# Kernel tuning notes

Measured on AMD Instinct MI355X. Metric: run time of the kernel, lower is better.

The kernel has to match this reference:

```python
import jax, jax.numpy as jnp
import numpy as np

B, D, CIN, H, W = 2, 6, 3, 96, 96
DIM, NUM_HEADS, DEPTH = 144, 6, 2
WS = (2, 8, 8)   # window size (d, h, w)
SS = (1, 4, 4)   # shift size for odd blocks
HID = int(DIM * 2.0)
TBL = (2 * WS[0] - 1) * (2 * WS[1] - 1) * (2 * WS[2] - 1)  # 675
EPS = 1e-5


def _rpi(ws):
    # pairwise relative position index, same math as WindowAttention.get_position_index
    coords = np.stack(np.meshgrid(np.arange(ws[0]), np.arange(ws[1]), np.arange(ws[2]), indexing='ij'))
    cf = coords.reshape(3, -1).astype(np.int64)
    rc = (cf[:, :, None] - cf[:, None, :]).transpose(1, 2, 0)
    rc[..., 0] += ws[0] - 1
    rc[..., 1] += ws[1] - 1
    rc[..., 2] += ws[2] - 1
    rc[..., 0] *= (2 * ws[1] - 1) * (2 * ws[2] - 1)
    rc[..., 1] *= 2 * ws[2] - 1
    return rc.sum(-1)  # (N, N)


def _win_part_np(x, ws):
    b, d, h, w, c = x.shape
    x = x.reshape(b, d // ws[0], ws[0], h // ws[1], ws[1], w // ws[2], ws[2], c)
    return x.transpose(0, 1, 3, 5, 2, 4, 6, 7).reshape(-1, ws[0] * ws[1] * ws[2], c)


def _attn_mask(Dp, Hp, Wp, ws, ss):
    # static shift-window attention mask, same as compute_mask
    img = np.zeros((1, Dp, Hp, Wp, 1), np.float32)
    cnt = 0
    for d in (slice(-ws[0]), slice(-ws[0], -ss[0]), slice(-ss[0], None)):
        for h in (slice(-ws[1]), slice(-ws[1], -ss[1]), slice(-ss[1], None)):
            for w in (slice(-ws[2]), slice(-ws[2], -ss[2]), slice(-ss[2], None)):
                img[:, d, h, w, :] = cnt
                cnt += 1
    mw = _win_part_np(img, ws)[..., 0]  # (nW, N)
    am = mw[:, None, :] - mw[:, :, None]
    return np.where(am != 0, np.float32(-100.0), np.float32(0.0))


RPI = jnp.asarray(_rpi(WS))            # (N, N) int
MASK = jnp.asarray(_attn_mask(D, H, W, WS, SS))  # (nW, N, N)


def _ln(x, g, b):
    mu = jnp.mean(x, -1, keepdims=True)
    var = jnp.mean(jnp.square(x - mu), -1, keepdims=True)
    return (x - mu) * jax.lax.rsqrt(var + EPS) * g + b


def _win_part(x, ws):
    b, d, h, w, c = x.shape
    x = x.reshape(b, d // ws[0], ws[0], h // ws[1], ws[1], w // ws[2], ws[2], c)
    return x.transpose(0, 1, 3, 5, 2, 4, 6, 7).reshape(-1, ws[0] * ws[1] * ws[2], c)


def _win_rev(xw, ws, b, d, h, w):
    x = xw.reshape(b, d // ws[0], h // ws[1], w // ws[2], ws[0], ws[1], ws[2], -1)
    return x.transpose(0, 1, 4, 2, 5, 3, 6, 7).reshape(b, d, h, w, -1)


def _stl(x, i, shifted, params):
    # one Swin Transformer Layer; x: (B, D, H, W, C)
    n1g, n1b, qkvw, qkvb, rpb, projw, projb, n2g, n2b, fc1w, fc1b, fc2w, fc2b = params
    b, d, h, w, c = x.shape
    hd = c // NUM_HEADS
    scale = hd ** -0.5
    y = _ln(x, n1g[i], n1b[i])
    if shifted:
        y = jnp.roll(y, (-SS[0], -SS[1], -SS[2]), axis=(1, 2, 3))
    xw = _win_part(y, WS)  # (B_, N, C)
    B_, N, _ = xw.shape
    qkv = jnp.einsum('bnc,oc->bno', xw, qkvw[i]) + qkvb[i]
    qkv = qkv.reshape(B_, N, 3, NUM_HEADS, hd).transpose(2, 0, 3, 1, 4)
    q, k, v = qkv[0], qkv[1], qkv[2]
    attn = jnp.einsum('bhnd,bhmd->bhnm', q * scale, k)
    bias = rpb[i][RPI].transpose(2, 0, 1)  # (heads, N, N)
    attn = attn + bias[None]
    if shifted:
        nW = MASK.shape[0]
        attn = attn.reshape(B_ // nW, nW, NUM_HEADS, N, N) + MASK[None, :, None]
        attn = attn.reshape(B_, NUM_HEADS, N, N)
    attn = jax.nn.softmax(attn, axis=-1)
    out = jnp.einsum('bhnm,bhmd->bhnd', attn, v).transpose(0, 2, 1, 3).reshape(B_, N, c)
    out = jnp.einsum('bnc,oc->bno', out, projw[i]) + projb[i]
    y = _win_rev(out, WS, b, d, h, w)
    if shifted:
        y = jnp.roll(y, (SS[0], SS[1], SS[2]), axis=(1, 2, 3))
    x = x + y
    z = _ln(x, n2g[i], n2b[i])
    z = jnp.einsum('bdhwc,oc->bdhwo', z, fc1w[i]) + fc1b[i]
    z = jax.nn.gelu(z, approximate=False)
    z = jnp.einsum('bdhwo,co->bdhwc', z, fc2w[i]) + fc2b[i]
    return x + z


def setup_inputs() -> dict:
    key = jax.random.key(0)
    ks = jax.random.split(key, 8)
    s = 0.02
    return {
        'x': jax.random.normal(ks[0], (B, D, CIN, H, W), jnp.float32),
        'conv_w': jax.random.normal(ks[1], (DIM, CIN, 1, 3, 3), jnp.float32) * s,
        'conv_b': jnp.zeros((DIM,), jnp.float32),
        'ln0_g': jnp.ones((DIM,), jnp.float32),
        'ln0_b': jnp.zeros((DIM,), jnp.float32),
        'n1g': jnp.ones((DEPTH, DIM), jnp.float32),
        'n1b': jnp.zeros((DEPTH, DIM), jnp.float32),
        'qkvw': jax.random.normal(ks[2], (DEPTH, 3 * DIM, DIM), jnp.float32) * s,
        'qkvb': jnp.zeros((DEPTH, 3 * DIM), jnp.float32),
        'rpb': jax.random.normal(ks[3], (DEPTH, TBL, NUM_HEADS), jnp.float32) * s,
        'projw': jax.random.normal(ks[4], (DEPTH, DIM, DIM), jnp.float32) * s,
        'projb': jnp.zeros((DEPTH, DIM), jnp.float32),
        'n2g': jnp.ones((DEPTH, DIM), jnp.float32),
        'n2b': jnp.zeros((DEPTH, DIM), jnp.float32),
        'fc1w': jax.random.normal(ks[5], (DEPTH, HID, DIM), jnp.float32) * s,
        'fc1b': jnp.zeros((DEPTH, HID), jnp.float32),
        'fc2w': jax.random.normal(ks[6], (DEPTH, DIM, HID), jnp.float32) * s,
        'fc2b': jnp.zeros((DEPTH, DIM), jnp.float32),
        'lin_w': jax.random.normal(ks[7], (DIM, DIM), jnp.float32) * s,
        'lin_b': jnp.zeros((DIM,), jnp.float32),
        'ln1_g': jnp.ones((DIM,), jnp.float32),
        'ln1_b': jnp.zeros((DIM,), jnp.float32),
    }


def reference(x, conv_w, conv_b, ln0_g, ln0_b, n1g, n1b, qkvw, qkvb, rpb, projw, projb,
              n2g, n2b, fc1w, fc1b, fc2w, fc2b, lin_w, lin_b, ln1_g, ln1_b):
    # x: (n, d, c, h, w)
    y = x.transpose(0, 2, 1, 3, 4)  # n c d h w
    y = jax.lax.conv_general_dilated(
        y, conv_w, (1, 1, 1), [(0, 0), (1, 1), (1, 1)],
        dimension_numbers=('NCDHW', 'OIDHW', 'NCDHW')) + conv_b[None, :, None, None, None]
    y = y.transpose(0, 2, 3, 4, 1)  # n d h w c
    y = _ln(y, ln0_g, ln0_b)
    y = y.transpose(0, 4, 1, 2, 3)  # n c d h w
    params = (n1g, n1b, qkvw, qkvb, rpb, projw, projb, n2g, n2b, fc1w, fc1b, fc2w, fc2b)
    # RSTB (num_blocks = 1): residual group (STG of DEPTH STLs) + linear + skip
    f = y.transpose(0, 2, 3, 4, 1)  # b d h w c
    for i in range(DEPTH):
        f = _stl(f, i, i % 2 == 1, params)
    f = jnp.einsum('bdhwc,oc->bdhwo', f, lin_w) + lin_b
    y = y + f.transpose(0, 4, 1, 2, 3)
    # trailing LayerNorm and rearrange back to (n, d, c, h, w)
    out = _ln(y.transpose(0, 2, 3, 4, 1), ln1_g, ln1_b)
    return out.transpose(0, 1, 4, 2, 3)
```

## Files before the change

### kernel.cpp

```cpp
#include <hip/hip_runtime.h>
#include <math.h>

#define NTOK 110592
#define NWIN 864
#define TS   15925248

typedef unsigned short u16;
typedef unsigned int   u32;
typedef __attribute__((ext_vector_type(8))) short short8;
typedef __attribute__((ext_vector_type(4))) float float4v;

__device__ __forceinline__ float bf2f(u16 v) { return __uint_as_float(((u32)v) << 16); }
__device__ __forceinline__ u16 f2bf(float f) {
    u32 u = __float_as_uint(f);
    u32 r = u + 0x7fffu + ((u >> 16) & 1u);
    return (u16)(r >> 16);
}
__device__ __forceinline__ void unpack2(u32 u, float& lo, float& hi) {
    lo = __uint_as_float(u << 16);
    hi = __uint_as_float(u & 0xffff0000u);
}
__device__ __forceinline__ u32 pack2(float lo, float hi) {
    return (u32)f2bf(lo) | ((u32)f2bf(hi) << 16);
}
__device__ __forceinline__ float wave_sum(float v) {
    #pragma unroll
    for (int o = 32; o > 0; o >>= 1) v += __shfl_xor(v, o, 64);
    return v;
}

__device__ __forceinline__ void win_to_src(int tw, int shifted, int& sb, int& sd, int& sh, int& sw) {
    int n = tw & 127;
    int win = tw >> 7;
    int ww = win % 12;
    int wh = (win / 12) % 12;
    int rest = win / 144;
    int wd = rest % 3;
    sb = rest / 3;
    int ld = n >> 6, lh = (n >> 3) & 7, lw = n & 7;
    int dr = wd * 2 + ld, hr = wh * 8 + lh, wr = ww * 8 + lw;
    if (shifted) {
        sd = (dr + 1) % 6;
        sh = (hr + 4) % 96;
        sw = (wr + 4) % 96;
    } else {
        sd = dr; sh = hr; sw = wr;
    }
}

__device__ __forceinline__ int tok_region(int t, int wdn, int whn, int wwn) {
    int dr = wdn * 2 + (t >> 6), hr = whn * 8 + ((t >> 3) & 7), wr = wwn * 8 + (t & 7);
    int rd = (dr < 4) ? 0 : ((dr < 5) ? 1 : 2);
    int rh = (hr < 88) ? 0 : ((hr < 92) ? 1 : 2);
    int rw = (wr < 88) ? 0 : ((wr < 92) ? 1 : 2);
    return rd * 9 + rh * 3 + rw;
}

__global__ __launch_bounds__(256) void convert_weights(
    const float* __restrict__ qkvw, const float* __restrict__ projw,
    const float* __restrict__ fc1w, const float* __restrict__ fc2w,
    const float* __restrict__ linw, u16* __restrict__ wbuf,
    const float* __restrict__ rpb, float* __restrict__ bexp)
{
    int i = blockIdx.x * 256 + threadIdx.x;
    if (i < 124416) wbuf[i] = f2bf(qkvw[i]);
    else if (i < 165888) wbuf[i] = f2bf(projw[i - 124416]);
    else if (i < 248832) wbuf[i] = f2bf(fc1w[i - 165888]);
    else if (i < 331776) wbuf[i] = f2bf(fc2w[i - 248832]);
    else if (i < 352512) wbuf[i] = f2bf(linw[i - 331776]);
    else if (i < 549120) {
        int k = i - 352512;
        int n = k & 127, m = (k >> 7) & 127;
        int lh = k >> 14;
        int h = lh % 6, l = lh / 6;
        int rdi = (m >> 6) - (n >> 6) + 1;
        int rhi = ((m >> 3) & 7) - ((n >> 3) & 7) + 7;
        int rwi = (m & 7) - (n & 7) + 7;
        int bi = (rdi * 15 + rhi) * 15 + rwi;
        bexp[k] = rpb[l * 4050 + bi * 6 + h];
    }
}

__global__ __launch_bounds__(256) void conv_ln0_row(
    const float* __restrict__ x, const float* __restrict__ cw, const float* __restrict__ cb,
    const float* __restrict__ g0, const float* __restrict__ b0,
    float* __restrict__ y0)
{
    int bh = blockIdx.x;
    int h = bh % 96, bd = bh / 96;
    int b = bd / 6, d = bd - b * 6;
    __shared__ float ws[192][29];
    __shared__ float xsr[9][100];
    __shared__ float cbias[192], gg[144], bbv[144];
    int tid = threadIdx.x;

    for (int i = tid; i < 9 * 98; i += 256) {
        int row = i / 98, wx = i - row * 98;
        int ci = row / 3, kh = row - 3 * ci;
        int hh = h + kh - 1, wsrc = wx - 1;
        float v = 0.f;
        if (hh >= 0 && hh < 96 && wsrc >= 0 && wsrc < 96)
            v = x[((((size_t)b * 6 + d) * 3 + ci) * 96 + hh) * 96 + wsrc];
        xsr[row][wx] = v;
    }
    for (int i = tid; i < 192 * 27; i += 256) {
        int c = i / 27, j = i - c * 27;
        ws[c][j] = (c < 144) ? cw[c * 27 + j] : 0.f;
    }
    for (int i = tid; i < 192; i += 256) cbias[i] = (i < 144) ? cb[i] : 0.f;
    for (int i = tid; i < 144; i += 256) { gg[i] = g0[i]; bbv[i] = b0[i]; }
    __syncthreads();

    int wv = tid >> 6, lane = tid & 63;
    int p0 = wv * 24;

    float a0[24], a1[24], a2[24];
    #pragma unroll
    for (int k = 0; k < 24; k++) {
        a0[k] = cbias[lane]; a1[k] = cbias[lane + 64]; a2[k] = cbias[lane + 128];
    }

    for (int cikh = 0; cikh < 9; cikh++) {
        const float* xr = &xsr[cikh][p0];
        float xv[26];
        #pragma unroll
        for (int t = 0; t < 26; t++) xv[t] = xr[t];
        #pragma unroll
        for (int kw = 0; kw < 3; kw++) {
            int j = cikh * 3 + kw;
            float w0 = ws[lane][j], w1 = ws[lane + 64][j], w2 = ws[lane + 128][j];
            #pragma unroll
            for (int k = 0; k < 24; k++) {
                float xvv = xv[k + kw];
                a0[k] += w0 * xvv; a1[k] += w1 * xvv; a2[k] += w2 * xvv;
            }
        }
    }

    #pragma unroll
    for (int k = 0; k < 24; k++) {
        int p = p0 + k;
        float v0 = a0[k], v1 = a1[k];
        float v2m = (lane < 16) ? a2[k] : 0.f;
        float s  = wave_sum(v0 + v1 + v2m);
        float s2 = wave_sum(v0 * v0 + v1 * v1 + v2m * v2m);
        float mu = s * (1.f / 144.f);
        float rstd = rsqrtf(fmaxf(s2 * (1.f / 144.f) - mu * mu, 0.f) + 1e-5f);
        size_t o = ((size_t)bh * 96 + p) * 144;
        float r0 = (v0 - mu) * rstd * gg[lane] + bbv[lane];
        float r1 = (v1 - mu) * rstd * gg[lane + 64] + bbv[lane + 64];
        y0[o + lane] = r0;
        y0[o + lane + 64] = r1;
        if (lane < 16) {
            float r2 = (a2[k] - mu) * rstd * gg[lane + 128] + bbv[lane + 128];
            y0[o + lane + 128] = r2;
        }
    }
}

template<int MODE>
__global__ __launch_bounds__(256) void ln_gather(
    const float* __restrict__ in, u16* __restrict__ out,
    const float* __restrict__ g, const float* __restrict__ bt)
{
    int tok = blockIdx.x * 4 + (threadIdx.x >> 6);
    int lane = threadIdx.x & 63;
    int src;
    if (MODE == 0) src = tok;
    else {
        int b, d, h, w;
        win_to_src(tok, MODE == 2, b, d, h, w);
        src = ((b * 6 + d) * 96 + h) * 96 + w;
    }
    const float* row = in + (size_t)src * 144;
    float v0 = row[lane], v1 = row[lane + 64], v2 = (lane < 16) ? row[lane + 128] : 0.f;
    float s  = wave_sum(v0 + v1 + v2);
    float s2 = wave_sum(v0 * v0 + v1 * v1 + v2 * v2);
    float mu = s * (1.f / 144.f);
    float rstd = rsqrtf(fmaxf(s2 * (1.f / 144.f) - mu * mu, 0.f) + 1e-5f);
    u16* orow = out + (size_t)tok * 144;
    orow[lane]      = f2bf((v0 - mu) * rstd * g[lane]      + bt[lane]);
    orow[lane + 64] = f2bf((v1 - mu) * rstd * g[lane + 64] + bt[lane + 64]);
    if (lane < 16)
        orow[lane + 128] = f2bf((v2 - mu) * rstd * g[lane + 128] + bt[lane + 128]);
}

template<int AMODE, int EPI, int SHIFTED, int ADDBIAS, int KTILES>
__global__ __launch_bounds__(192) void mgemm(
    const void* __restrict__ Asrc, const u16* __restrict__ Wt, const float* __restrict__ bias,
    u16* __restrict__ outb, float* __restrict__ fres, const float* __restrict__ y0,
    int a_add, int a_ld, int w_ld, int o_ld, int o_add)
{
    __shared__ u16 As[64 * 152];
    int m0 = blockIdx.y * 64, n0 = blockIdx.x * 144;
    int tid = threadIdx.x;
    int wv3 = tid / 64, lane = tid & 63;
    int mrow = lane & 15, quad = lane >> 4;
    const short8 z8 = {0, 0, 0, 0, 0, 0, 0, 0};

    float4v acc[4][3];
    #pragma unroll
    for (int i = 0; i < 4; i++)
        #pragma unroll
        for (int j = 0; j < 3; j++) acc[i][j] = (float4v){0.f, 0.f, 0.f, 0.f};

    #pragma unroll
    for (int kt = 0; kt < KTILES; kt++) {
        if (kt) __syncthreads();
        if (AMODE == 2) {
            const u16* A = (const u16*)Asrc;
            #pragma unroll
            for (int idx = tid; idx < 1152; idx += 192) {
                int r = idx / 18, c4 = idx - r * 18;
                *(short8*)&As[r * 152 + c4 * 8] =
                    *(const short8*)&A[(size_t)(a_add + m0 + r) * a_ld + kt * 144 + c4 * 8];
            }
        } else {
            const float* A = (const float*)Asrc;
            #pragma unroll
            for (int idx = tid; idx < 2304; idx += 192) {
                int r = idx / 36, c4 = idx - r * 36;
                const float4* src4 = (const float4*)&A[(size_t)(a_add + m0 + r) * a_ld + kt * 144];
                float4 v = src4[c4];
                *(u32*)&As[r * 152 + c4 * 4]     = pack2(v.x, v.y);
                *(u32*)&As[r * 152 + c4 * 4 + 2] = pack2(v.z, v.w);
            }
        }
        __syncthreads();

        const u16* Wg = Wt + (size_t)(n0 + wv3 * 48 + mrow) * w_ld + kt * 144;

        #pragma unroll
        for (int ks = 0; ks < 4; ks++) {
            int k0 = ks * 32;
            short8 af[4], bf[3];
            #pragma unroll
            for (int i = 0; i < 4; i++)
                af[i] = *(const short8*)&As[(i * 16 + mrow) * 152 + k0 + quad * 8];
            #pragma unroll
            for (int j = 0; j < 3; j++)
                bf[j] = *(const short8*)&Wg[(size_t)j * 16 * w_ld + k0 + quad * 8];
            #pragma unroll
            for (int i = 0; i < 4; i++)
                #pragma unroll
                for (int j = 0; j < 3; j++)
                    acc[i][j] = __builtin_amdgcn_mfma_f32_16x16x32_bf16(af[i], bf[j], acc[i][j], 0, 0, 0);
        }
        {
            bool tl = (quad < 2);
            short8 af[4], bf[3];
            #pragma unroll
            for (int i = 0; i < 4; i++)
                af[i] = tl ? *(const short8*)&As[(i * 16 + mrow) * 152 + 128 + quad * 8] : z8;
            #pragma unroll
            for (int j = 0; j < 3; j++)
                bf[j] = tl ? *(const short8*)&Wg[(size_t)j * 16 * w_ld + 128 + quad * 8] : z8;
            #pragma unroll
            for (int i = 0; i < 4; i++)
                #pragma unroll
                for (int j = 0; j < 3; j++)
                    acc[i][j] = __builtin_amdgcn_mfma_f32_16x16x32_bf16(af[i], bf[j], acc[i][j], 0, 0, 0);
        }
    }

    #pragma unroll
    for (int i = 0; i < 4; i++) {
        #pragma unroll
        for (int reg = 0; reg < 4; reg++) {
            int m = m0 + i * 16 + quad * 4 + reg;
            int orow;
            if (EPI == 2 || EPI == 5) {
                int b, d, h, w;
                win_to_src(m, SHIFTED, b, d, h, w);
                orow = ((b * 6 + d) * 96 + h) * 96 + w;
            } else orow = m + o_add;
            #pragma unroll
            for (int j = 0; j < 3; j++) {
                int n = n0 + wv3 * 48 + j * 16 + mrow;
                float v = acc[i][j][reg];
                if (ADDBIAS) v += bias[n];
                if (EPI == 1) v = 0.5f * v * (1.f + erff(v * 0.70710678118f));
                if (EPI == 2 || EPI == 3) {
                    fres[(size_t)orow * 144 + n] += v;
                } else if (EPI == 5) {
                    fres[(size_t)orow * 144 + n] = y0[(size_t)orow * 144 + n] + v;
                } else if (EPI == 6) {
                    int slot = n / 144;
                    int hn = n - slot * 144;
                    int head = hn / 24, dd = hn - head * 24;
                    if (slot == 0) v *= 0.20412414523193154f;
                    outb[((size_t)head * o_ld + orow) * 72 + slot * 24 + dd] = f2bf(v);
                } else {
                    if (EPI == 4) v += y0[(size_t)orow * o_ld + n];
                    outb[(size_t)orow * o_ld + n] = f2bf(v);
                }
            }
        }
    }
}

template<int SHIFTED>
__global__ __launch_bounds__(256) void attn_mfma(
    const u16* __restrict__ qkv,
    const float* __restrict__ bexp,
    u16* __restrict__ tok_out, int win_base, int chtok)
{
    int win = blockIdx.x;
    int head = blockIdx.y;
    __shared__ __align__(16) u16 Pb[4][16][152];
    __shared__ __align__(16) u16 Vt[24][152];
    __shared__ float invden_s[128];
    __shared__ u32 reg_pack[32];

    int tid = threadIdx.x;
    int wv = tid >> 6, lane = tid & 63;
    int c = lane & 15, quad = lane >> 4;
    int qbase = wv * 32;
    const short8 z8 = {0, 0, 0, 0, 0, 0, 0, 0};
    const float* bh_ = bexp + head * 16384;
    const u16* base = qkv + ((size_t)head * chtok + (size_t)win * 128) * 72;

    int wdn = 0, whn = 0, wwn = 0;
    if (SHIFTED) {
        int wib = (win_base + win) % 432;
        wwn = wib % 12; whn = (wib / 12) % 12; wdn = wib / 144;
    }

    if (tid < 128) {
        const u32* vsrc = (const u32*)(base + (size_t)tid * 72 + 48);
        #pragma unroll
        for (int i = 0; i < 12; i++) {
            u32 u = vsrc[i];
            Vt[2 * i][tid]     = (u16)(u & 0xffffu);
            Vt[2 * i + 1][tid] = (u16)(u >> 16);
        }
    }
    if (SHIFTED && tid < 32) {
        int t0 = tid * 4;
        reg_pack[tid] = (u32)tok_region(t0, wdn, whn, wwn)
                      | ((u32)tok_region(t0 + 1, wdn, whn, wwn) << 8)
                      | ((u32)tok_region(t0 + 2, wdn, whn, wwn) << 16)
                      | ((u32)tok_region(t0 + 3, wdn, whn, wwn) << 24);
    }
    __syncthreads();

    short8 aq[2];
    #pragma unroll
    for (int i = 0; i < 2; i++) {
        aq[i] = z8;
        if (quad < 3)
            aq[i] = *(const short8*)(base + (size_t)(qbase + i * 16 + c) * 72 + quad * 8);
    }

    float4v s_acc[2][8];
    #pragma unroll
    for (int i = 0; i < 2; i++)
        #pragma unroll
        for (int j = 0; j < 8; j++) s_acc[i][j] = (float4v){0.f, 0.f, 0.f, 0.f};

    #pragma unroll
    for (int j = 0; j < 8; j++) {
        short8 kf = z8;
        if (quad < 3)
            kf = *(const short8*)(base + (size_t)(j * 16 + c) * 72 + 24 + quad * 8);
        s_acc[0][j] = __builtin_amdgcn_mfma_f32_16x16x32_bf16(kf, aq[0], s_acc[0][j], 0, 0, 0);
        s_acc[1][j] = __builtin_amdgcn_mfma_f32_16x16x32_bf16(kf, aq[1], s_acc[1][j], 0, 0, 0);
    }

    float4v o_acc[2][2];
    #pragma unroll
    for (int i = 0; i < 2; i++)
        #pragma unroll
        for (int jv = 0; jv < 2; jv++) o_acc[i][jv] = (float4v){0.f, 0.f, 0.f, 0.f};

    #pragma unroll
    for (int i = 0; i < 2; i++) {
        int m = qbase + i * 16 + c;
        const float* brow = bh_ + m * 128;
        u32 myreg = SHIFTED ? (u32)tok_region(m, wdn, whn, wwn) : 0u;
        float den = 0.f;
        #pragma unroll
        for (int j = 0; j < 8; j++) {
            float4 bv = *(const float4*)(brow + j * 16 + quad * 4);
            float s0 = s_acc[i][j][0] + bv.x;
            float s1 = s_acc[i][j][1] + bv.y;
            float s2 = s_acc[i][j][2] + bv.z;
            float s3 = s_acc[i][j][3] + bv.w;
            if (SHIFTED) {
                u32 rv = reg_pack[j * 4 + quad];
                s0 += ((rv & 255u) == myreg) ? 0.f : -100.f;
                s1 += (((rv >> 8) & 255u) == myreg) ? 0.f : -100.f;
                s2 += (((rv >> 16) & 255u) == myreg) ? 0.f : -100.f;
                s3 += ((rv >> 24) == myreg) ? 0.f : -100.f;
            }
            float p0 = __expf(s0), p1 = __expf(s1), p2 = __expf(s2), p3 = __expf(s3);
            den += (p0 + p1) + (p2 + p3);
            u32 w0, w1;
            asm("v_cvt_pk_bf16_f32 %0, %1, %2" : "=v"(w0) : "v"(p0), "v"(p1));
            asm("v_cvt_pk_bf16_f32 %0, %1, %2" : "=v"(w1) : "v"(p2), "v"(p3));
            uint2 wpair = make_uint2(w0, w1);
            *(uint2*)&Pb[wv][c][j * 16 + quad * 4] = wpair;
        }
        den += __shfl_xor(den, 16, 64);
        den += __shfl_xor(den, 32, 64);
        if (quad == 0) invden_s[m] = 1.f / den;

        #pragma unroll
        for (int ks = 0; ks < 4; ks++) {
            short8 pf  = *(const short8*)&Pb[wv][c][ks * 32 + quad * 8];
            short8 vf0 = *(const short8*)&Vt[c][ks * 32 + quad * 8];
            short8 vf1 = (c < 8) ? *(const short8*)&Vt[16 + c][ks * 32 + quad * 8] : z8;
            o_acc[i][0] = __builtin_amdgcn_mfma_f32_16x16x32_bf16(pf, vf0, o_acc[i][0], 0, 0, 0);
            o_acc[i][1] = __builtin_amdgcn_mfma_f32_16x16x32_bf16(pf, vf1, o_acc[i][1], 0, 0, 0);
        }
    }

    float* ob = (float*)&Pb[wv][0][0];
    #pragma unroll
    for (int i = 0; i < 2; i++)
        #pragma unroll
        for (int jv = 0; jv < 2; jv++) {
            int d = jv * 16 + c;
            if (d < 24) {
                #pragma unroll
                for (int r = 0; r < 4; r++)
                    ob[(i * 16 + quad * 4 + r) * 26 + d] = o_acc[i][jv][r];
            }
        }
    __syncthreads();

    if (tid < 128) {
        const float2* ol = (const float2*)((const float*)&Pb[0][0][0]
                                           + (tid >> 5) * 1216 + (tid & 31) * 26);
        float inv = invden_s[tid];
        u32* orow = (u32*)tok_out + ((size_t)((win_base + win) * 128 + tid)) * 72 + head * 12;
        #pragma unroll
        for (int d2 = 0; d2 < 12; d2++) {
            float2 v = ol[d2];
            orow[d2] = pack2(v.x * inv, v.y * inv);
        }
    }
}

__global__ __launch_bounds__(256) void final_ln_out_kernel(
    const u16* __restrict__ gsrc, const float* __restrict__ g, const float* __restrict__ bt,
    float* __restrict__ out)
{
    int bh = blockIdx.x;
    int h = bh % 96, d = (bh / 96) % 6, b = bh / 576;
    __shared__ u16 tile[96][152];
    __shared__ float stat[96][2];
    const u16* src = gsrc + (size_t)bh * 96 * 144;
    for (int i = threadIdx.x; i < 1728; i += 256) {
        int wt = i / 18, c8 = i - wt * 18;
        *(short8*)&tile[wt][c8 * 8] = *(const short8*)&src[wt * 144 + c8 * 8];
    }
    __syncthreads();
    if (threadIdx.x < 96) {
        const u32* row = (const u32*)&tile[threadIdx.x][0];
        float s = 0.f, s2 = 0.f;
        #pragma unroll
        for (int j = 0; j < 72; j++) {
            float lo, hi; unpack2(row[j], lo, hi);
            s += lo + hi; s2 += lo * lo + hi * hi;
        }
        float mu = s * (1.f / 144.f);
        float var = s2 * (1.f / 144.f) - mu * mu;
        stat[threadIdx.x][0] = mu;
        stat[threadIdx.x][1] = rsqrtf(fmaxf(var, 0.f) + 1e-5f);
    }
    __syncthreads();
    size_t obase = ((size_t)(b * 6 + d) * 144) * 9216 + h * 96;
    for (int i = threadIdx.x; i < 96 * 144; i += blockDim.x) {
        int c = i / 96, wt = i - c * 96;
        out[obase + (size_t)c * 9216 + wt] =
            (bf2f(tile[wt][c]) - stat[wt][0]) * stat[wt][1] * g[c] + bt[c];
    }
}

extern "C" void kernel_launch(void* const* d_in, const int* in_sizes, int n_in,
                              void* d_out, int out_size, void* d_ws, size_t ws_size,
                              hipStream_t stream) {
    const float* x     = (const float*)d_in[0];
    const float* convw = (const float*)d_in[1];
    const float* convb = (const float*)d_in[2];
    const float* ln0g  = (const float*)d_in[3];
    const float* ln0b  = (const float*)d_in[4];
    const float* n1g   = (const float*)d_in[5];
    const float* n1b   = (const float*)d_in[6];
    const float* qkvw  = (const float*)d_in[7];
    const float* qkvb  = (const float*)d_in[8];
    const float* rpb   = (const float*)d_in[9];
    const float* projw = (const float*)d_in[10];
    const float* projb = (const float*)d_in[11];
    const float* n2g   = (const float*)d_in[12];
    const float* n2b   = (const float*)d_in[13];
    const float* fc1w  = (const float*)d_in[14];
    const float* fc1b  = (const float*)d_in[15];
    const float* fc2w  = (const float*)d_in[16];
    const float* fc2b  = (const float*)d_in[17];
    const float* linw  = (const float*)d_in[18];
    const float* linb  = (const float*)d_in[19];
    const float* ln1g  = (const float*)d_in[20];
    const float* ln1b  = (const float*)d_in[21];

    char* wp = (char*)d_ws;
    float* f    = (float*)wp;             wp += (size_t)TS * 4;
    u16*   tok  = (u16*)wp;               wp += (size_t)TS * 2;
    u16*   wbuf = (u16*)wp;               wp += 352512ull * 2;
    float* bexp = (float*)wp;             wp += 196608ull * 4;
    u16*   qkvbuf = (u16*)wp;
    size_t rest = ws_size - (size_t)(wp - (char*)d_ws);
    int nch = (rest >= (size_t)NTOK * 432 * 2) ? 1
            : (rest >= (size_t)NTOK * 216 * 2) ? 2 : 4;
    int nm  = (rest >= (size_t)NTOK * 288 * 2) ? 1
            : (rest >= (size_t)NTOK * 144 * 2) ? 2 : 3;
    float* y0 = (float*)d_out;

    convert_weights<<<2145, 256, 0, stream>>>(qkvw, projw, fc1w, fc2w, linw, wbuf, rpb, bexp);
    conv_ln0_row<<<1152, 256, 0, stream>>>(x, convw, convb, ln0g, ln0b, y0);

    for (int layer = 0; layer < 2; ++layer) {
        const u16* qw  = wbuf + (size_t)layer * 62208;
        const u16* pw  = wbuf + 124416 + (size_t)layer * 20736;
        const u16* f1w = wbuf + 165888 + (size_t)layer * 41472;
        const u16* f2w = wbuf + 248832 + (size_t)layer * 41472;
        const float* qb  = qkvb + (size_t)layer * 432;
        const float* pb  = projb + (size_t)layer * 144;
        const float* g1  = n1g + layer * 144;
        const float* b1  = n1b + layer * 144;
        const float* g2  = n2g + layer * 144;
        const float* b2  = n2b + layer * 144;
        const float* f1b = fc1b + (size_t)layer * 288;
        const float* f2b = fc2b + (size_t)layer * 144;
        const float* bx  = bexp + (size_t)layer * 98304;

        if (layer == 0) ln_gather<1><<<NTOK / 4, 256, 0, stream>>>(y0, tok, g1, b1);
        else            ln_gather<2><<<NTOK / 4, 256, 0, stream>>>(f, tok, g1, b1);

        int chtok = NTOK / nch, chwin = NWIN / nch;
        for (int c = 0; c < nch; c++) {
            mgemm<2, 6, 0, 1, 1><<<dim3(3, chtok / 64), 192, 0, stream>>>(
                tok, qw, qb, qkvbuf, nullptr, nullptr,
                c * chtok, 144, 144, chtok, 0);
            if (layer == 0)
                attn_mfma<0><<<dim3(chwin, 6), 256, 0, stream>>>(qkvbuf, bx, tok, c * chwin, chtok);
            else
                attn_mfma<1><<<dim3(chwin, 6), 256, 0, stream>>>(qkvbuf, bx, tok, c * chwin, chtok);
        }

        if (layer == 0)
            mgemm<2, 5, 0, 1, 1><<<dim3(1, NTOK / 64), 192, 0, stream>>>(
                tok, pw, pb, nullptr, f, y0, 0, 144, 144, 144, 0);
        else
            mgemm<2, 2, 1, 1, 1><<<dim3(1, NTOK / 64), 192, 0, stream>>>(
                tok, pw, pb, nullptr, f, nullptr, 0, 144, 144, 144, 0);

        ln_gather<0><<<NTOK / 4, 256, 0, stream>>>(f, tok, g2, b2);

        int fcch = NTOK / nm;
        for (int c = 0; c < nm; c++) {
            int mst = c * fcch;
            mgemm<2, 1, 0, 1, 1><<<dim3(2, fcch / 64), 192, 0, stream>>>(
                tok, f1w, f1b, qkvbuf, nullptr, nullptr, mst, 144, 144, 288, 0);
            mgemm<2, 3, 0, 1, 2><<<dim3(1, fcch / 64), 192, 0, stream>>>(
                qkvbuf, f2w, f2b, nullptr, f, nullptr, 0, 288, 288, 144, mst);
        }
    }

    mgemm<0, 4, 0, 1, 1><<<dim3(1, NTOK / 64), 192, 0, stream>>>(
        f, wbuf + 331776, linb, tok, nullptr, y0, 0, 144, 144, 144, 0);

    final_ln_out_kernel<<<2 * 6 * 96, 256, 0, stream>>>(tok, ln1g, ln1b, (float*)d_out);
}
```

Before: 806.4 us.

## Write V transposed from QKV GEMM epilogue and vectorize LayerNorm gather

The QKV GEMM epilogue now stores Q/K in a packed 48-wide per-head layout and writes V directly in a per-window transposed layout. The attention kernel then reads V fragments straight from global memory instead of transposing V through shared memory, and the unshifted variant no longer needs a block barrier. Separately, the LayerNorm gather loads rows as float2 and stores packed bf16 pairs. The trade-off is scattered 2-byte stores for V in the GEMM epilogue and uncached global loads of V in attention.

```diff
diff --git a/kernel.cpp b/kernel.cpp
--- a/kernel.cpp
+++ b/kernel.cpp
@@ -172,17 +172,22 @@
         win_to_src(tok, MODE == 2, b, d, h, w);
         src = ((b * 6 + d) * 96 + h) * 96 + w;
     }
-    const float* row = in + (size_t)src * 144;
-    float v0 = row[lane], v1 = row[lane + 64], v2 = (lane < 16) ? row[lane + 128] : 0.f;
-    float s  = wave_sum(v0 + v1 + v2);
-    float s2 = wave_sum(v0 * v0 + v1 * v1 + v2 * v2);
+    const float2* row = (const float2*)(in + (size_t)src * 144);
+    float2 a = row[lane];
+    float2 b2 = (lane < 8) ? row[64 + lane] : make_float2(0.f, 0.f);
+    float s  = wave_sum(a.x + a.y + b2.x + b2.y);
+    float s2 = wave_sum(a.x * a.x + a.y * a.y + b2.x * b2.x + b2.y * b2.y);
     float mu = s * (1.f / 144.f);
     float rstd = rsqrtf(fmaxf(s2 * (1.f / 144.f) - mu * mu, 0.f) + 1e-5f);
-    u16* orow = out + (size_t)tok * 144;
-    orow[lane]      = f2bf((v0 - mu) * rstd * g[lane]      + bt[lane]);
-    orow[lane + 64] = f2bf((v1 - mu) * rstd * g[lane + 64] + bt[lane + 64]);
-    if (lane < 16)
-        orow[lane + 128] = f2bf((v2 - mu) * rstd * g[lane + 128] + bt[lane + 128]);
+    const float2* g2 = (const float2*)g;
+    const float2* t2 = (const float2*)bt;
+    u32* orow = (u32*)(out + (size_t)tok * 144);
+    float2 gg = g2[lane], tt = t2[lane];
+    orow[lane] = pack2((a.x - mu) * rstd * gg.x + tt.x, (a.y - mu) * rstd * gg.y + tt.y);
+    if (lane < 8) {
+        float2 gh = g2[64 + lane], th = t2[64 + lane];
+        orow[64 + lane] = pack2((b2.x - mu) * rstd * gh.x + th.x, (b2.y - mu) * rstd * gh.y + th.y);
+    }
 }
 
 template<int AMODE, int EPI, int SHIFTED, int ADDBIAS, int KTILES>
@@ -288,8 +293,16 @@
                     int slot = n / 144;
                     int hn = n - slot * 144;
                     int head = hn / 24, dd = hn - head * 24;
-                    if (slot == 0) v *= 0.20412414523193154f;
-                    outb[((size_t)head * o_ld + orow) * 72 + slot * 24 + dd] = f2bf(v);
+                    if (slot == 0) {
+                        v *= 0.20412414523193154f;
+                        outb[((size_t)head * o_ld + orow) * 48 + dd] = f2bf(v);
+                    } else if (slot == 1) {
+                        outb[((size_t)head * o_ld + orow) * 48 + 24 + dd] = f2bf(v);
+                    } else {
+                        u16* vt = (u16*)fres;
+                        vt[(((size_t)head * (o_ld >> 7) + (orow >> 7)) * 24 + dd) * 128
+                           + (orow & 127)] = f2bf(v);
+                    }
                 } else {
                     if (EPI == 4) v += y0[(size_t)orow * o_ld + n];
                     outb[(size_t)orow * o_ld + n] = f2bf(v);
@@ -301,14 +314,13 @@
 
 template<int SHIFTED>
 __global__ __launch_bounds__(256) void attn_mfma(
-    const u16* __restrict__ qkv,
+    const u16* __restrict__ qk, const u16* __restrict__ vt,
     const float* __restrict__ bexp,
     u16* __restrict__ tok_out, int win_base, int chtok)
 {
     int win = blockIdx.x;
     int head = blockIdx.y;
     __shared__ __align__(16) u16 Pb[4][16][152];
-    __shared__ __align__(16) u16 Vt[24][152];
     __shared__ float invden_s[128];
     __shared__ u32 reg_pack[32];
 
@@ -318,38 +330,29 @@
     int qbase = wv * 32;
     const short8 z8 = {0, 0, 0, 0, 0, 0, 0, 0};
     const float* bh_ = bexp + head * 16384;
-    const u16* base = qkv + ((size_t)head * chtok + (size_t)win * 128) * 72;
+    const u16* base = qk + ((size_t)head * chtok + (size_t)win * 128) * 48;
+    const u16* vtw  = vt + ((size_t)head * (chtok >> 7) + win) * 3072;
 
     int wdn = 0, whn = 0, wwn = 0;
     if (SHIFTED) {
         int wib = (win_base + win) % 432;
         wwn = wib % 12; whn = (wib / 12) % 12; wdn = wib / 144;
-    }
-
-    if (tid < 128) {
-        const u32* vsrc = (const u32*)(base + (size_t)tid * 72 + 48);
-        #pragma unroll
-        for (int i = 0; i < 12; i++) {
-            u32 u = vsrc[i];
-            Vt[2 * i][tid]     = (u16)(u & 0xffffu);
-            Vt[2 * i + 1][tid] = (u16)(u >> 16);
-        }
-    }
-    if (SHIFTED && tid < 32) {
-        int t0 = tid * 4;
-        reg_pack[tid] = (u32)tok_region(t0, wdn, whn, wwn)
-                      | ((u32)tok_region(t0 + 1, wdn, whn, wwn) << 8)
-                      | ((u32)tok_region(t0 + 2, wdn, whn, wwn) << 16)
-                      | ((u32)tok_region(t0 + 3, wdn, whn, wwn) << 24);
-    }
-    __syncthreads();
+        if (tid < 32) {
+            int t0 = tid * 4;
+            reg_pack[tid] = (u32)tok_region(t0, wdn, whn, wwn)
+                          | ((u32)tok_region(t0 + 1, wdn, whn, wwn) << 8)
+                          | ((u32)tok_region(t0 + 2, wdn, whn, wwn) << 16)
+                          | ((u32)tok_region(t0 + 3, wdn, whn, wwn) << 24);
+        }
+        __syncthreads();
+    }
 
     short8 aq[2];
     #pragma unroll
     for (int i = 0; i < 2; i++) {
         aq[i] = z8;
         if (quad < 3)
-            aq[i] = *(const short8*)(base + (size_t)(qbase + i * 16 + c) * 72 + quad * 8);
+            aq[i] = *(const short8*)(base + (size_t)(qbase + i * 16 + c) * 48 + quad * 8);
     }
 
     float4v s_acc[2][8];
@@ -362,7 +365,7 @@
     for (int j = 0; j < 8; j++) {
         short8 kf = z8;
         if (quad < 3)
-            kf = *(const short8*)(base + (size_t)(j * 16 + c) * 72 + 24 + quad * 8);
+            kf = *(const short8*)(base + (size_t)(j * 16 + c) * 48 + 24 + quad * 8);
         s_acc[0][j] = __builtin_amdgcn_mfma_f32_16x16x32_bf16(kf, aq[0], s_acc[0][j], 0, 0, 0);
         s_acc[1][j] = __builtin_amdgcn_mfma_f32_16x16x32_bf16(kf, aq[1], s_acc[1][j], 0, 0, 0);
     }
@@ -408,8 +411,8 @@
         #pragma unroll
         for (int ks = 0; ks < 4; ks++) {
             short8 pf  = *(const short8*)&Pb[wv][c][ks * 32 + quad * 8];
-            short8 vf0 = *(const short8*)&Vt[c][ks * 32 + quad * 8];
-            short8 vf1 = (c < 8) ? *(const short8*)&Vt[16 + c][ks * 32 + quad * 8] : z8;
+            short8 vf0 = *(const short8*)&vtw[c * 128 + ks * 32 + quad * 8];
+            short8 vf1 = (c < 8) ? *(const short8*)&vtw[(16 + c) * 128 + ks * 32 + quad * 8] : z8;
             o_acc[i][0] = __builtin_amdgcn_mfma_f32_16x16x32_bf16(pf, vf0, o_acc[i][0], 0, 0, 0);
             o_acc[i][1] = __builtin_amdgcn_mfma_f32_16x16x32_bf16(pf, vf1, o_acc[i][1], 0, 0, 0);
         }
@@ -539,14 +542,15 @@
         else            ln_gather<2><<<NTOK / 4, 256, 0, stream>>>(f, tok, g1, b1);
 
         int chtok = NTOK / nch, chwin = NWIN / nch;
+        u16* vtb = qkvbuf + (size_t)288 * chtok;
         for (int c = 0; c < nch; c++) {
             mgemm<2, 6, 0, 1, 1><<<dim3(3, chtok / 64), 192, 0, stream>>>(
-                tok, qw, qb, qkvbuf, nullptr, nullptr,
+                tok, qw, qb, qkvbuf, (float*)vtb, nullptr,
                 c * chtok, 144, 144, chtok, 0);
             if (layer == 0)
-                attn_mfma<0><<<dim3(chwin, 6), 256, 0, stream>>>(qkvbuf, bx, tok, c * chwin, chtok);
+                attn_mfma<0><<<dim3(chwin, 6), 256, 0, stream>>>(qkvbuf, vtb, bx, tok, c * chwin, chtok);
             else
-                attn_mfma<1><<<dim3(chwin, 6), 256, 0, stream>>>(qkvbuf, bx, tok, c * chwin, chtok);
+                attn_mfma<1><<<dim3(chwin, 6), 256, 0, stream>>>(qkvbuf, vtb, bx, tok, c * chwin, chtok);
         }
 
         if (layer == 0)
```

Measured after the change: 909.8 us. 12.8% more time.

## Reuse staged A tile across N blocks, swizzle attention LDS, vectorize LayerNorm

Applied to the files above, without the earlier changes.

The GEMM kernel gains an NB template parameter. The QKV and FC1 GEMMs now stage the A tile into shared memory once per block and loop over all 144-wide output column blocks, instead of launching one block per column block. This removes redundant global reads of A at the cost of fewer, longer-running blocks. The attention kernel replaces its padded P/V shared-memory arrays with XOR-swizzled dense layouts to avoid bank conflicts and shrink LDS use. LayerNorm gather now uses float2 loads and packed bf16 stores.

```diff
diff --git a/kernel.cpp b/kernel.cpp
--- a/kernel.cpp
+++ b/kernel.cpp
@@ -172,44 +172,49 @@
         win_to_src(tok, MODE == 2, b, d, h, w);
         src = ((b * 6 + d) * 96 + h) * 96 + w;
     }
-    const float* row = in + (size_t)src * 144;
-    float v0 = row[lane], v1 = row[lane + 64], v2 = (lane < 16) ? row[lane + 128] : 0.f;
-    float s  = wave_sum(v0 + v1 + v2);
-    float s2 = wave_sum(v0 * v0 + v1 * v1 + v2 * v2);
+    const float2* row = (const float2*)(in + (size_t)src * 144);
+    float2 a = row[lane];
+    float2 b2 = (lane < 8) ? row[64 + lane] : make_float2(0.f, 0.f);
+    float s  = wave_sum(a.x + a.y + b2.x + b2.y);
+    float s2 = wave_sum(a.x * a.x + a.y * a.y + b2.x * b2.x + b2.y * b2.y);
     float mu = s * (1.f / 144.f);
     float rstd = rsqrtf(fmaxf(s2 * (1.f / 144.f) - mu * mu, 0.f) + 1e-5f);
-    u16* orow = out + (size_t)tok * 144;
-    orow[lane]      = f2bf((v0 - mu) * rstd * g[lane]      + bt[lane]);
-    orow[lane + 64] = f2bf((v1 - mu) * rstd * g[lane + 64] + bt[lane + 64]);
-    if (lane < 16)
-        orow[lane + 128] = f2bf((v2 - mu) * rstd * g[lane + 128] + bt[lane + 128]);
-}
-
-template<int AMODE, int EPI, int SHIFTED, int ADDBIAS, int KTILES>
+    const float2* g2 = (const float2*)g;
+    const float2* t2 = (const float2*)bt;
+    u32* orow = (u32*)(out + (size_t)tok * 144);
+    float2 gg = g2[lane], tt = t2[lane];
+    orow[lane] = pack2((a.x - mu) * rstd * gg.x + tt.x, (a.y - mu) * rstd * gg.y + tt.y);
+    if (lane < 8) {
+        float2 gh = g2[64 + lane], th = t2[64 + lane];
+        orow[64 + lane] = pack2((b2.x - mu) * rstd * gh.x + th.x, (b2.y - mu) * rstd * gh.y + th.y);
+    }
+}
+
+template<int AMODE, int EPI, int SHIFTED, int ADDBIAS, int KTILES, int NB>
 __global__ __launch_bounds__(192) void mgemm(
     const void* __restrict__ Asrc, const u16* __restrict__ Wt, const float* __restrict__ bias,
     u16* __restrict__ outb, float* __restrict__ fres, const float* __restrict__ y0,
     int a_add, int a_ld, int w_ld, int o_ld, int o_add)
 {
     __shared__ u16 As[64 * 152];
-    int m0 = blockIdx.y * 64, n0 = blockIdx.x * 144;
+    int m0 = blockIdx.y * 64;
     int tid = threadIdx.x;
     int wv3 = tid / 64, lane = tid & 63;
     int mrow = lane & 15, quad = lane >> 4;
     const short8 z8 = {0, 0, 0, 0, 0, 0, 0, 0};
 
     float4v acc[4][3];
-    #pragma unroll
-    for (int i = 0; i < 4; i++)
-        #pragma unroll
-        for (int j = 0; j < 3; j++) acc[i][j] = (float4v){0.f, 0.f, 0.f, 0.f};
-
-    #pragma unroll
-    for (int kt = 0; kt < KTILES; kt++) {
-        if (kt) __syncthreads();
+
+    auto zero_acc = [&]() {
+        #pragma unroll
+        for (int i = 0; i < 4; i++)
+            #pragma unroll
+            for (int j = 0; j < 3; j++) acc[i][j] = (float4v){0.f, 0.f, 0.f, 0.f};
+    };
+
+    auto stageA = [&](int kt) {
         if (AMODE == 2) {
             const u16* A = (const u16*)Asrc;
-            #pragma unroll
             for (int idx = tid; idx < 1152; idx += 192) {
                 int r = idx / 18, c4 = idx - r * 18;
                 *(short8*)&As[r * 152 + c4 * 8] =
@@ -217,7 +222,6 @@
             }
         } else {
             const float* A = (const float*)Asrc;
-            #pragma unroll
             for (int idx = tid; idx < 2304; idx += 192) {
                 int r = idx / 36, c4 = idx - r * 36;
                 const float4* src4 = (const float4*)&A[(size_t)(a_add + m0 + r) * a_ld + kt * 144];
@@ -226,10 +230,10 @@
                 *(u32*)&As[r * 152 + c4 * 4 + 2] = pack2(v.z, v.w);
             }
         }
-        __syncthreads();
-
+    };
+
+    auto mfma_tile = [&](int n0, int kt) {
         const u16* Wg = Wt + (size_t)(n0 + wv3 * 48 + mrow) * w_ld + kt * 144;
-
         #pragma unroll
         for (int ks = 0; ks < 4; ks++) {
             int k0 = ks * 32;
@@ -261,40 +265,63 @@
                 for (int j = 0; j < 3; j++)
                     acc[i][j] = __builtin_amdgcn_mfma_f32_16x16x32_bf16(af[i], bf[j], acc[i][j], 0, 0, 0);
         }
-    }
-
-    #pragma unroll
-    for (int i = 0; i < 4; i++) {
-        #pragma unroll
-        for (int reg = 0; reg < 4; reg++) {
-            int m = m0 + i * 16 + quad * 4 + reg;
-            int orow;
-            if (EPI == 2 || EPI == 5) {
-                int b, d, h, w;
-                win_to_src(m, SHIFTED, b, d, h, w);
-                orow = ((b * 6 + d) * 96 + h) * 96 + w;
-            } else orow = m + o_add;
-            #pragma unroll
-            for (int j = 0; j < 3; j++) {
-                int n = n0 + wv3 * 48 + j * 16 + mrow;
-                float v = acc[i][j][reg];
-                if (ADDBIAS) v += bias[n];
-                if (EPI == 1) v = 0.5f * v * (1.f + erff(v * 0.70710678118f));
-                if (EPI == 2 || EPI == 3) {
-                    fres[(size_t)orow * 144 + n] += v;
-                } else if (EPI == 5) {
-                    fres[(size_t)orow * 144 + n] = y0[(size_t)orow * 144 + n] + v;
-                } else if (EPI == 6) {
-                    int slot = n / 144;
-                    int hn = n - slot * 144;
-                    int head = hn / 24, dd = hn - head * 24;
-                    if (slot == 0) v *= 0.20412414523193154f;
-                    outb[((size_t)head * o_ld + orow) * 72 + slot * 24 + dd] = f2bf(v);
-                } else {
-                    if (EPI == 4) v += y0[(size_t)orow * o_ld + n];
-                    outb[(size_t)orow * o_ld + n] = f2bf(v);
+    };
+
+    auto epilogue = [&](int n0) {
+        #pragma unroll
+        for (int i = 0; i < 4; i++) {
+            #pragma unroll
+            for (int reg = 0; reg < 4; reg++) {
+                int m = m0 + i * 16 + quad * 4 + reg;
+                int orow;
+                if (EPI == 2 || EPI == 5) {
+                    int b, d, h, w;
+                    win_to_src(m, SHIFTED, b, d, h, w);
+                    orow = ((b * 6 + d) * 96 + h) * 96 + w;
+                } else orow = m + o_add;
+                #pragma unroll
+                for (int j = 0; j < 3; j++) {
+                    int n = n0 + wv3 * 48 + j * 16 + mrow;
+                    float v = acc[i][j][reg];
+                    if (ADDBIAS) v += bias[n];
+                    if (EPI == 1) v = 0.5f * v * (1.f + erff(v * 0.70710678118f));
+                    if (EPI == 2 || EPI == 3) {
+                        fres[(size_t)orow * 144 + n] += v;
+                    } else if (EPI == 5) {
+                        fres[(size_t)orow * 144 + n] = y0[(size_t)orow * 144 + n] + v;
+                    } else if (EPI == 6) {
+                        int slot = n / 144;
+                        int hn = n - slot * 144;
+                        int head = hn / 24, dd = hn - head * 24;
+                        if (slot == 0) v *= 0.20412414523193154f;
+                        outb[((size_t)head * o_ld + orow) * 72 + slot * 24 + dd] = f2bf(v);
+                    } else {
+                        if (EPI == 4) v += y0[(size_t)orow * o_ld + n];
+                        outb[(size_t)orow * o_ld + n] = f2bf(v);
+                    }
                 }
             }
+        }
+    };
+
+    if (NB == 1) {
+        zero_acc();
+        #pragma unroll
+        for (int kt = 0; kt < KTILES; kt++) {
+            if (kt) __syncthreads();
+            stageA(kt);
+            __syncthreads();
+            mfma_tile(0, kt);
+        }
+        epilogue(0);
+    } else {
+        stageA(0);
+        __syncthreads();
+        #pragma unroll
+        for (int nb = 0; nb < NB; nb++) {
+            zero_acc();
+            mfma_tile(nb * 144, 0);
+            epilogue(nb * 144);
         }
     }
 }
@@ -307,8 +334,8 @@
 {
     int win = blockIdx.x;
     int head = blockIdx.y;
-    __shared__ __align__(16) u16 Pb[4][16][152];
-    __shared__ __align__(16) u16 Vt[24][152];
+    __shared__ __align__(16) u16 Pb[4][2048];
+    __shared__ __align__(16) u16 Vt[3072];
     __shared__ float invden_s[128];
     __shared__ u32 reg_pack[32];
 
@@ -319,6 +346,7 @@
     const short8 z8 = {0, 0, 0, 0, 0, 0, 0, 0};
     const float* bh_ = bexp + head * 16384;
     const u16* base = qkv + ((size_t)head * chtok + (size_t)win * 128) * 72;
+    int cs = (c & 7) << 3;
 
     int wdn = 0, whn = 0, wwn = 0;
     if (SHIFTED) {
@@ -331,8 +359,9 @@
         #pragma unroll
         for (int i = 0; i < 12; i++) {
             u32 u = vsrc[i];
-            Vt[2 * i][tid]     = (u16)(u & 0xffffu);
-            Vt[2 * i + 1][tid] = (u16)(u >> 16);
+            int d0 = 2 * i, d1 = 2 * i + 1;
+            Vt[((d0 << 7) + tid) ^ ((d0 & 7) << 3)] = (u16)(u & 0xffffu);
+            Vt[((d1 << 7) + tid) ^ ((d1 & 7) << 3)] = (u16)(u >> 16);
         }
     }
     if (SHIFTED && tid < 32) {
@@ -399,7 +428,7 @@
             asm("v_cvt_pk_bf16_f32 %0, %1, %2" : "=v"(w0) : "v"(p0), "v"(p1));
             asm("v_cvt_pk_bf16_f32 %0, %1, %2" : "=v"(w1) : "v"(p2), "v"(p3));
             uint2 wpair = make_uint2(w0, w1);
-            *(uint2*)&Pb[wv][c][j * 16 + quad * 4] = wpair;
+            *(uint2*)&Pb[wv][((c << 7) + j * 16 + quad * 4) ^ cs] = wpair;
         }
         den += __shfl_xor(den, 16, 64);
         den += __shfl_xor(den, 32, 64);
@@ -407,15 +436,15 @@
 
         #pragma unroll
         for (int ks = 0; ks < 4; ks++) {
-            short8 pf  = *(const short8*)&Pb[wv][c][ks * 32 + quad * 8];
-            short8 vf0 = *(const short8*)&Vt[c][ks * 32 + quad * 8];
-            short8 vf1 = (c < 8) ? *(const short8*)&Vt[16 + c][ks * 32 + quad * 8] : z8;
+            short8 pf  = *(const short8*)&Pb[wv][((c << 7) + ks * 32 + quad * 8) ^ cs];
+            short8 vf0 = *(const short8*)&Vt[((c << 7) + ks * 32 + quad * 8) ^ cs];
+            short8 vf1 = (c < 8) ? *(const short8*)&Vt[(((16 + c) << 7) + ks * 32 + quad * 8) ^ cs] : z8;
             o_acc[i][0] = __builtin_amdgcn_mfma_f32_16x16x32_bf16(pf, vf0, o_acc[i][0], 0, 0, 0);
             o_acc[i][1] = __builtin_amdgcn_mfma_f32_16x16x32_bf16(pf, vf1, o_acc[i][1], 0, 0, 0);
         }
     }
 
-    float* ob = (float*)&Pb[wv][0][0];
+    float* ob = (float*)&Pb[wv][0];
     #pragma unroll
     for (int i = 0; i < 2; i++)
         #pragma unroll
@@ -430,8 +459,8 @@
     __syncthreads();
 
     if (tid < 128) {
-        const float2* ol = (const float2*)((const float*)&Pb[0][0][0]
-                                           + (tid >> 5) * 1216 + (tid & 31) * 26);
+        const float2* ol = (const float2*)((const float*)&Pb[0][0]
+                                           + (tid >> 5) * 1024 + (tid & 31) * 26);
         float inv = invden_s[tid];
         u32* orow = (u32*)tok_out + ((size_t)((win_base + win) * 128 + tid)) * 72 + head * 12;
         #pragma unroll
@@ -540,7 +569,7 @@
 
         int chtok = NTOK / nch, chwin = NWIN / nch;
         for (int c = 0; c < nch; c++) {
-            mgemm<2, 6, 0, 1, 1><<<dim3(3, chtok / 64), 192, 0, stream>>>(
+            mgemm<2, 6, 0, 1, 1, 3><<<dim3(1, chtok / 64), 192, 0, stream>>>(
                 tok, qw, qb, qkvbuf, nullptr, nullptr,
                 c * chtok, 144, 144, chtok, 0);
             if (layer == 0)
@@ -550,10 +579,10 @@
         }
 
         if (layer == 0)
-            mgemm<2, 5, 0, 1, 1><<<dim3(1, NTOK / 64), 192, 0, stream>>>(
+            mgemm<2, 5, 0, 1, 1, 1><<<dim3(1, NTOK / 64), 192, 0, stream>>>(
                 tok, pw, pb, nullptr, f, y0, 0, 144, 144, 144, 0);
         else
-            mgemm<2, 2, 1, 1, 1><<<dim3(1, NTOK / 64), 192, 0, stream>>>(
+            mgemm<2, 2, 1, 1, 1, 1><<<dim3(1, NTOK / 64), 192, 0, stream>>>(
                 tok, pw, pb, nullptr, f, nullptr, 0, 144, 144, 144, 0);
 
         ln_gather<0><<<NTOK / 4, 256, 0, stream>>>(f, tok, g2, b2);
@@ -561,14 +590,14 @@
         int fcch = NTOK / nm;
         for (int c = 0; c < nm; c++) {
             int mst = c * fcch;
-            mgemm<2, 1, 0, 1, 1><<<dim3(2, fcch / 64), 192, 0, stream>>>(
+            mgemm<2, 1, 0, 1, 1, 2><<<dim3(1, fcch / 64), 192, 0, stream>>>(
                 tok, f1w, f1b, qkvbuf, nullptr, nullptr, mst, 144, 144, 288, 0);
-            mgemm<2, 3, 0, 1, 2><<<dim3(1, fcch / 64), 192, 0, stream>>>(
+            mgemm<2, 3, 0, 1, 2, 1><<<dim3(1, fcch / 64), 192, 0, stream>>>(
                 qkvbuf, f2w, f2b, nullptr, f, nullptr, 0, 288, 288, 144, mst);
         }
     }
 
-    mgemm<0, 4, 0, 1, 1><<<dim3(1, NTOK / 64), 192, 0, stream>>>(
+    mgemm<0, 4, 0, 1, 1, 1><<<dim3(1, NTOK / 64), 192, 0, stream>>>(
         f, wbuf + 331776, linb, tok, nullptr, y0, 0, 144, 144, 144, 0);
 
     final_ln_out_kernel<<<2 * 6 * 96, 256, 0, stream>>>(tok, ln1g, ln1b, (float*)d_out);
```

New measurement: 852.6 us. 5.7% more time.
